# Optimization experiments

Measured on AMD Instinct MI355X. Metric: run time of the kernel, lower is better.

The kernel has to match this reference:

```python
import jax, jax.numpy as jnp
import numpy as np

B, LQ, LD, H, DIM, PF = 16, 64, 2048, 1024, 128, 4
MAXK = LD // PF + 1  # static upper bound on num clusters (valid_len <= LD)


def setup_inputs() -> dict:
    key = jax.random.key(0)
    k1, k2, k3, k4 = jax.random.split(key, 4)
    return {
        "q_hidden": jax.random.normal(k1, (B, LQ, H), jnp.float32),
        "d_hidden": jax.random.normal(k2, (B, LD, H), jnp.float32),
        "W": jax.random.normal(k3, (H, DIM), jnp.float32) * (1.0 / np.sqrt(H)),  # xavier-ish
        "b": jnp.zeros((DIM,), jnp.float32),
        "q_mask": jnp.ones((B, LQ), jnp.int32),
        "d_mask": jnp.ones((B, LD), jnp.int32),
        "labels": jax.random.randint(k4, (B, LD), 0, MAXK, dtype=jnp.int32),
        "pooling_factor": PF,
    }


def _encode(hidden, W, b, mask):
    # proj -> L2 normalize -> zero out padded tokens
    r = hidden @ W + b
    r = r / jnp.clip(jnp.linalg.norm(r, axis=-1, keepdims=True), 1e-12)
    return r * mask[..., None].astype(r.dtype)


def _pool(d_repr, d_mask, labels, pf):
    # segment-mean per batch sample, cluster labels supplied externally
    Bn, L, D = d_repr.shape
    max_k = L // pf + 1  # static
    valid = jnp.clip(d_mask.sum(-1), 2, None)          # [B]
    k = valid // pf + 1                                 # per-sample num clusters
    lab = jnp.where(d_mask > 0, labels % k[:, None], max_k)  # invalid tokens -> dummy seg
    seg = lambda vals, idx: jax.ops.segment_sum(vals, idx, num_segments=max_k + 1)
    sums = jax.vmap(seg)(d_repr, lab)[:, :max_k]                          # [B,K,D]
    counts = jax.vmap(seg)(jnp.where(d_mask > 0, 1.0, 0.0), lab)[:, :max_k]
    means = sums / jnp.clip(counts, 1.0)[..., None]
    means = means / jnp.clip(jnp.linalg.norm(means, axis=-1, keepdims=True), 1e-12)
    pad_mask = jnp.arange(max_k)[None, :] < k[:, None]                    # [B,K]
    return means * pad_mask[..., None], pad_mask


def reference(q_hidden, d_hidden, W, b, q_mask, d_mask, labels, pooling_factor):
    q = _encode(q_hidden, W, b, q_mask)            # [B,LQ,DIM]
    d = _encode(d_hidden, W, b, d_mask)            # [B,LD,DIM]
    d_pool, pmask = _pool(d, d_mask, labels, pooling_factor)  # [B,K,DIM]
    sim = jnp.einsum('bqd,bkd->bqk', q, d_pool)
    sim = jnp.where(pmask[:, None, :], sim, -1e4)
    score = (sim.max(-1) * q_mask.astype(sim.dtype)).sum(-1)  # maxsum per pair
    return score
```

## Files before the change

### kernel.cpp

```cpp
#include <hip/hip_runtime.h>
#include <hip/hip_bf16.h>

#define BB    16
#define LQ    64
#define LD    2048
#define HH    1024
#define DIM   128
#define MAXK  513
#define SCH   9
#define DGRID 512
#define QGRID 16

typedef __attribute__((ext_vector_type(8))) short short8;
typedef __attribute__((ext_vector_type(4))) float f32x4;

__device__ __forceinline__ float b2f(ushort u) {
    union { float f; unsigned int u32; } c; c.u32 = ((unsigned int)u) << 16; return c.f;
}
__device__ __forceinline__ ushort f2b_rn(float f) {
    unsigned int x = __float_as_uint(f);
    return (ushort)((x + 0x7fffu + ((x >> 16) & 1u)) >> 16);
}

__device__ __forceinline__ void gld16(void* lds, const void* g) {
    __builtin_amdgcn_global_load_lds(
        (const __attribute__((address_space(1))) unsigned int*)g,
        (__attribute__((address_space(3))) unsigned int*)lds,
        16, 0, 0);
}

__global__ __launch_bounds__(256) void prep_kb_kernel(
    const float* __restrict__ W,
    const int*   __restrict__ d_mask,
    const int*   __restrict__ pf,
    ushort*      __restrict__ Wt,
    int*         __restrict__ kvals,
    float*       __restrict__ sums)
{
    int bid = blockIdx.x, t = threadIdx.x;
    if (bid < 16) {
        __shared__ ushort tile[128][72];
        const int h0 = bid * 64;
        #pragma unroll
        for (int i = 0; i < 32; ++i) {
            int flat = i * 256 + t;
            int r = flat >> 7, c = flat & 127;
            tile[c][r] = f2b_rn(W[(long)(h0 + r) * DIM + c]);
        }
        __syncthreads();
        #pragma unroll
        for (int i = 0; i < 4; ++i) {
            int flat = i * 256 + t;
            int n = flat >> 3, u = flat & 7;
            uint4 v = *(const uint4*)&tile[n][u * 8];
            *(uint4*)&Wt[(long)n * HH + h0 + u * 8] = v;
        }
    } else if (bid < 32) {
        __shared__ int red[4];
        int b = bid - 16;
        int lane = t & 63, wave = t >> 6;
        int s = 0;
        for (int i = t; i < LD; i += 256) s += (d_mask[b * LD + i] > 0) ? 1 : 0;
        #pragma unroll
        for (int m = 1; m < 64; m <<= 1) s += __shfl_xor(s, m);
        if (lane == 0) red[wave] = s;
        __syncthreads();
        if (t == 0) {
            int v = red[0] + red[1] + red[2] + red[3];
            if (v < 2) v = 2;
            int pfv = pf[0];
            if (pfv < 1 || pfv > LD) pfv = 4;
            kvals[b] = v / pfv + 1;
        }
    } else {
        const int total4 = (BB * MAXK * DIM) / 4;
        float4* s4 = (float4*)sums;
        const float4 z = make_float4(0.f, 0.f, 0.f, 0.f);
        for (int i = (bid - 32) * 256 + t; i < total4; i += 256 * 256)
            s4[i] = z;
    }
}

__global__ __launch_bounds__(512, 6) void encode_kernel(
    const float*  __restrict__ Xd,
    const float*  __restrict__ Xq,
    const ushort* __restrict__ Wt,
    const float*  __restrict__ bias,
    const int*    __restrict__ mask_d,
    const int*    __restrict__ mask_q,
    const int*    __restrict__ labels,
    const int*    __restrict__ kvals,
    float*        __restrict__ sums,
    float*        __restrict__ q_repr)
{
    __shared__ __align__(16) uint4 buf[3][1024];
    __shared__ float ssh[64][2];

    const int bid = blockIdx.x;
    const bool isq = bid >= DGRID;
    const float* X = isq ? Xq : Xd;
    const long row0 = isq ? (long)(bid - DGRID) * 64 : (long)bid * 64;

    const int t = threadIdx.x;
    const int w = t >> 6, lane = t & 63;
    const int m16 = lane & 15, quad = lane >> 4;
    const int rh = w & 3, ch = w >> 2;

    const float*  gA = X + (row0 + w * 8 + (lane >> 3)) * HH
                         + (((lane & 7) ^ ((lane >> 3) & 7)) * 4);
    const ushort* gB = Wt + (long)(w * 16 + (lane >> 2)) * HH
                          + (((lane & 3) ^ ((lane >> 4) & 3)) * 8);

    const int wA = w * 64;
    const int wB = 512 + w * 64;

    f32x4 acc[4];
    #pragma unroll
    for (int j = 0; j < 4; ++j) acc[j] = (f32x4){0.f, 0.f, 0.f, 0.f};

    gld16(&buf[0][wA], gA);
    gld16(&buf[0][wB], gB);
    gld16(&buf[1][wA], gA + 32);
    gld16(&buf[1][wB], gB + 32);

    const int sw = m16 & 7;
    const int bsw = m16 >> 2;
    const int au = (rh * 16 + m16) * 8;

    auto compute = [&](const uint4* bb) {
        float4 va0 = *(const float4*)&bb[au + ((2 * quad) ^ sw)];
        float4 va1 = *(const float4*)&bb[au + ((2 * quad + 1) ^ sw)];
        float av[8];
        *(float4*)(av) = va0; *(float4*)(av + 4) = va1;
        short8 ah, al;
        #pragma unroll
        for (int j = 0; j < 8; ++j) {
            unsigned int ux = __float_as_uint(av[j]);
            ah[j] = (short)(ux >> 16);
            float hif = __uint_as_float(ux & 0xffff0000u);
            al[j] = (short)(__float_as_uint(av[j] - hif) >> 16);
        }
        #pragma unroll
        for (int cti = 0; cti < 4; ++cti) {
            const int ct = ch * 4 + cti;
            short8 bf = *(const short8*)&bb[512 + (ct * 16 + m16) * 4 + (quad ^ bsw)];
            acc[cti] = __builtin_amdgcn_mfma_f32_16x16x32_bf16(ah, bf, acc[cti], 0, 0, 0);
            acc[cti] = __builtin_amdgcn_mfma_f32_16x16x32_bf16(al, bf, acc[cti], 0, 0, 0);
        }
    };

    #define STEP(C, CUR, NXT)                                              \
        asm volatile("s_waitcnt vmcnt(2)" ::: "memory");                   \
        __builtin_amdgcn_s_barrier();                                      \
        __builtin_amdgcn_sched_barrier(0);                                 \
        gld16(&buf[NXT][wA], gA + ((C) + 2) * 32);                         \
        gld16(&buf[NXT][wB], gB + ((C) + 2) * 32);                         \
        compute(&buf[CUR][0]);

    for (int c = 0; c < 30; c += 3) {
        STEP(c + 0, 0, 2)
        STEP(c + 1, 1, 0)
        STEP(c + 2, 2, 1)
    }
    #undef STEP
    asm volatile("s_waitcnt vmcnt(2)" ::: "memory");
    __builtin_amdgcn_s_barrier();
    __builtin_amdgcn_sched_barrier(0);
    compute(&buf[0][0]);
    asm volatile("s_waitcnt vmcnt(0)" ::: "memory");
    __builtin_amdgcn_s_barrier();
    __builtin_amdgcn_sched_barrier(0);
    compute(&buf[1][0]);

    float bia[4];
    #pragma unroll
    for (int cti = 0; cti < 4; ++cti) bia[cti] = bias[(ch * 4 + cti) * 16 + m16];

    float vv[4][4];
    float ssp[4] = {0.f, 0.f, 0.f, 0.f};
    #pragma unroll
    for (int cti = 0; cti < 4; ++cti)
        #pragma unroll
        for (int r = 0; r < 4; ++r) {
            vv[cti][r] = acc[cti][r] + bia[cti];
            ssp[r] += vv[cti][r] * vv[cti][r];
        }
    #pragma unroll
    for (int r = 0; r < 4; ++r) {
        ssp[r] += __shfl_xor(ssp[r], 1);
        ssp[r] += __shfl_xor(ssp[r], 2);
        ssp[r] += __shfl_xor(ssp[r], 4);
        ssp[r] += __shfl_xor(ssp[r], 8);
    }
    if (m16 == 0) {
        #pragma unroll
        for (int r = 0; r < 4; ++r) ssh[rh * 16 + quad * 4 + r][ch] = ssp[r];
    }
    __syncthreads();

    #pragma unroll
    for (int r = 0; r < 4; ++r) {
        int rowl = rh * 16 + quad * 4 + r;
        long rowg = row0 + rowl;
        float ss = ssh[rowl][0] + ssh[rowl][1];
        float scale = 1.0f / fmaxf(sqrtf(ss), 1e-12f);
        if (isq) {
            scale *= (float)mask_q[rowg];
            #pragma unroll
            for (int cti = 0; cti < 4; ++cti)
                q_repr[rowg * DIM + (ch * 4 + cti) * 16 + m16] = vv[cti][r] * scale;
        } else if (mask_d[rowg] > 0) {
            int b = (int)(rowg >> 11);
            int seg = labels[rowg] % kvals[b];
            float* sp = sums + ((long)b * MAXK + seg) * DIM + m16;
            #pragma unroll
            for (int cti = 0; cti < 4; ++cti)
                atomicAdd(sp + (ch * 4 + cti) * 16, vv[cti][r] * scale);
        }
    }
}

__global__ __launch_bounds__(256) void simmax_kernel(
    const float* __restrict__ q_repr,
    const float* __restrict__ sums,
    const int*   __restrict__ kvals,
    float*       __restrict__ pmax)
{
    __shared__ __align__(16) ushort Qh[64 * 136];
    __shared__ __align__(16) ushort Ql[64 * 136];
    __shared__ __align__(16) ushort Ch[64 * 136];
    __shared__ float cn[64];

    int b = blockIdx.x / SCH, chunk = blockIdx.x % SCH;
    int t = threadIdx.x, w = t >> 6, lane = t & 63;
    int m16 = lane & 15, quad = lane >> 4;

    #pragma unroll
    for (int i = 0; i < 8; ++i) {
        int flat = i * 256 + t;
        int row = flat >> 5, c4 = flat & 31;
        float4 v = *(const float4*)(q_repr + ((long)b * LQ + row) * DIM + c4 * 4);
        float x[4]; *(float4*)x = v;
        ushort4 h, l;
        ushort* hp = (ushort*)&h; ushort* lp = (ushort*)&l;
        #pragma unroll
        for (int j = 0; j < 4; ++j) {
            unsigned int ux = __float_as_uint(x[j]);
            hp[j] = (ushort)(ux >> 16);
            lp[j] = f2b_rn(x[j] - __uint_as_float(ux & 0xffff0000u));
        }
        *(ushort4*)&Qh[row * 136 + c4 * 4] = h;
        *(ushort4*)&Ql[row * 136 + c4 * 4] = l;
    }
    #pragma unroll
    for (int i = 0; i < 8; ++i) {
        int flat = i * 256 + t;
        int row = flat >> 5, c4 = flat & 31;
        int kk = chunk * 64 + row;
        float4 v = (kk < MAXK)
            ? *(const float4*)(sums + ((long)b * MAXK + kk) * DIM + c4 * 4)
            : make_float4(0.f, 0.f, 0.f, 0.f);
        ushort4 h; ushort* hp = (ushort*)&h;
        hp[0] = f2b_rn(v.x); hp[1] = f2b_rn(v.y);
        hp[2] = f2b_rn(v.z); hp[3] = f2b_rn(v.w);
        *(ushort4*)&Ch[row * 136 + c4 * 4] = h;
    }
    __syncthreads();

    {
        int c = w * 16 + m16;
        float ssv = 0.f;
        #pragma unroll
        for (int j = 0; j < 16; ++j) {
            unsigned int u = *(const unsigned int*)&Ch[c * 136 + quad * 32 + j * 2];
            float x0 = b2f((ushort)u), x1 = b2f((ushort)(u >> 16));
            ssv += x0 * x0 + x1 * x1;
        }
        ssv += __shfl_xor(ssv, 16);
        ssv += __shfl_xor(ssv, 32);
        if (quad == 0) cn[c] = (ssv > 1e-24f) ? rsqrtf(ssv) : 0.f;
    }
    __syncthreads();

    f32x4 acc[4];
    #pragma unroll
    for (int j = 0; j < 4; ++j) acc[j] = (f32x4){0.f, 0.f, 0.f, 0.f};

    #pragma unroll
    for (int kc = 0; kc < 4; ++kc) {
        short8 qh = *(const short8*)&Qh[(w * 16 + m16) * 136 + kc * 32 + quad * 8];
        short8 ql = *(const short8*)&Ql[(w * 16 + m16) * 136 + kc * 32 + quad * 8];
        #pragma unroll
        for (int ct = 0; ct < 4; ++ct) {
            short8 cf = *(const short8*)&Ch[(ct * 16 + m16) * 136 + kc * 32 + quad * 8];
            acc[ct] = __builtin_amdgcn_mfma_f32_16x16x32_bf16(qh, cf, acc[ct], 0, 0, 0);
            acc[ct] = __builtin_amdgcn_mfma_f32_16x16x32_bf16(ql, cf, acc[ct], 0, 0, 0);
        }
    }

    int kb = kvals[b];
    #pragma unroll
    for (int r = 0; r < 4; ++r) {
        float mx = -1e4f;
        #pragma unroll
        for (int ct = 0; ct < 4; ++ct) {
            int cl = chunk * 64 + ct * 16 + m16;
            float sim = acc[ct][r] * cn[ct * 16 + m16];
            mx = fmaxf(mx, (cl < kb) ? sim : -1e4f);
        }
        mx = fmaxf(mx, __shfl_xor(mx, 1));
        mx = fmaxf(mx, __shfl_xor(mx, 2));
        mx = fmaxf(mx, __shfl_xor(mx, 4));
        mx = fmaxf(mx, __shfl_xor(mx, 8));
        if (m16 == 0)
            pmax[((long)b * SCH + chunk) * 64 + w * 16 + quad * 4 + r] = mx;
    }
}

__global__ __launch_bounds__(64) void final_kernel(
    const float* __restrict__ pmax,
    const int*   __restrict__ q_mask,
    float*       __restrict__ out)
{
    int b = blockIdx.x, r = threadIdx.x;
    float m = -3e38f;
    #pragma unroll
    for (int c = 0; c < SCH; ++c)
        m = fmaxf(m, pmax[((long)b * SCH + c) * 64 + r]);
    m *= (float)q_mask[b * LQ + r];
    #pragma unroll
    for (int sh = 1; sh < 64; sh <<= 1) m += __shfl_xor(m, sh);
    if (r == 0) out[b] = m;
}

extern "C" void kernel_launch(void* const* d_in, const int* in_sizes, int n_in,
                              void* d_out, int out_size, void* d_ws, size_t ws_size,
                              hipStream_t stream) {
    const float* q_hidden = (const float*)d_in[0];
    const float* d_hidden = (const float*)d_in[1];
    const float* W        = (const float*)d_in[2];
    const float* bias     = (const float*)d_in[3];
    const int*   q_mask   = (const int*)d_in[4];
    const int*   d_mask   = (const int*)d_in[5];
    const int*   labels   = (const int*)d_in[6];
    const int*   pf       = (const int*)d_in[7];

    float* ws     = (float*)d_ws;
    float* q_repr = ws;
    float* sums   = q_repr + (long)BB * LQ * DIM;
    float* pmaxb  = sums + (long)BB * MAXK * DIM;
    int*   kvals  = (int*)(pmaxb + BB * SCH * 64);
    ushort* Wt    = (ushort*)(kvals + 16);

    prep_kb_kernel<<<288, 256, 0, stream>>>(W, d_mask, pf, Wt, kvals, sums);
    encode_kernel<<<DGRID + QGRID, 512, 0, stream>>>(d_hidden, q_hidden, Wt, bias,
                                                     d_mask, q_mask, labels, kvals,
                                                     sums, q_repr);
    simmax_kernel<<<BB * SCH, 256, 0, stream>>>(q_repr, sums, kvals, pmaxb);
    final_kernel<<<BB, 64, 0, stream>>>(pmaxb, q_mask, (float*)d_out);
}
```

Measured before the change: 254.9 us.

## Restructure encode GEMM: per-wave 16-row units with full-width W staged in LDS

The encode kernel now gives each wave a 16-row unit that covers all 128 output columns. The block stages a quarter of the bf16 weight matrix in 64KB of LDS at a time, while A rows stream straight from global into a three-deep register prefetch instead of going through LDS. This lets each split-hi/lo conversion of A feed 8 column tiles instead of 4, and drops the cross-wave norm reduction through shared memory along with most barriers. In exchange, half the waves only help load W and do no math, LDS use grows, which may lower occupancy, and the direct global A loads are less coalesced.

Measured after the change: 247.0 us. 3.1% less time.

```diff
diff --git a/kernel.cpp b/kernel.cpp
--- a/kernel.cpp
+++ b/kernel.cpp
@@ -8,8 +8,8 @@
 #define DIM   128
 #define MAXK  513
 #define SCH   9
-#define DGRID 512
-#define QGRID 16
+#define NUNITS 2112
+#define EGRID 512
 
 typedef __attribute__((ext_vector_type(8))) short short8;
 typedef __attribute__((ext_vector_type(4))) float f32x4;
@@ -81,7 +81,7 @@
     }
 }
 
-__global__ __launch_bounds__(512, 6) void encode_kernel(
+__global__ __launch_bounds__(512, 4) void encode_kernel(
     const float*  __restrict__ Xd,
     const float*  __restrict__ Xq,
     const ushort* __restrict__ Wt,
@@ -93,97 +93,97 @@
     float*        __restrict__ sums,
     float*        __restrict__ q_repr)
 {
-    __shared__ __align__(16) uint4 buf[3][1024];
-    __shared__ float ssh[64][2];
-
-    const int bid = blockIdx.x;
-    const bool isq = bid >= DGRID;
-    const float* X = isq ? Xq : Xd;
-    const long row0 = isq ? (long)(bid - DGRID) * 64 : (long)bid * 64;
+    __shared__ __align__(16) uint4 Wlds[4096];
 
     const int t = threadIdx.x;
     const int w = t >> 6, lane = t & 63;
     const int m16 = lane & 15, quad = lane >> 4;
-    const int rh = w & 3, ch = w >> 2;
-
-    const float*  gA = X + (row0 + w * 8 + (lane >> 3)) * HH
-                         + (((lane & 7) ^ ((lane >> 3) & 7)) * 4);
-    const ushort* gB = Wt + (long)(w * 16 + (lane >> 2)) * HH
-                          + (((lane & 3) ^ ((lane >> 4) & 3)) * 8);
-
-    const int wA = w * 64;
-    const int wB = 512 + w * 64;
-
-    f32x4 acc[4];
-    #pragma unroll
-    for (int j = 0; j < 4; ++j) acc[j] = (f32x4){0.f, 0.f, 0.f, 0.f};
-
-    gld16(&buf[0][wA], gA);
-    gld16(&buf[0][wB], gB);
-    gld16(&buf[1][wA], gA + 32);
-    gld16(&buf[1][wB], gB + 32);
-
-    const int sw = m16 & 7;
-    const int bsw = m16 >> 2;
-    const int au = (rh * 16 + m16) * 8;
-
-    auto compute = [&](const uint4* bb) {
-        float4 va0 = *(const float4*)&bb[au + ((2 * quad) ^ sw)];
-        float4 va1 = *(const float4*)&bb[au + ((2 * quad + 1) ^ sw)];
-        float av[8];
-        *(float4*)(av) = va0; *(float4*)(av + 4) = va1;
-        short8 ah, al;
-        #pragma unroll
-        for (int j = 0; j < 8; ++j) {
-            unsigned int ux = __float_as_uint(av[j]);
-            ah[j] = (short)(ux >> 16);
-            float hif = __uint_as_float(ux & 0xffff0000u);
-            al[j] = (short)(__float_as_uint(av[j] - hif) >> 16);
-        }
-        #pragma unroll
-        for (int cti = 0; cti < 4; ++cti) {
-            const int ct = ch * 4 + cti;
-            short8 bf = *(const short8*)&bb[512 + (ct * 16 + m16) * 4 + (quad ^ bsw)];
-            acc[cti] = __builtin_amdgcn_mfma_f32_16x16x32_bf16(ah, bf, acc[cti], 0, 0, 0);
-            acc[cti] = __builtin_amdgcn_mfma_f32_16x16x32_bf16(al, bf, acc[cti], 0, 0, 0);
-        }
-    };
-
-    #define STEP(C, CUR, NXT)                                              \
-        asm volatile("s_waitcnt vmcnt(2)" ::: "memory");                   \
-        __builtin_amdgcn_s_barrier();                                      \
-        __builtin_amdgcn_sched_barrier(0);                                 \
-        gld16(&buf[NXT][wA], gA + ((C) + 2) * 32);                         \
-        gld16(&buf[NXT][wB], gB + ((C) + 2) * 32);                         \
-        compute(&buf[CUR][0]);
-
-    for (int c = 0; c < 30; c += 3) {
-        STEP(c + 0, 0, 2)
-        STEP(c + 1, 1, 0)
-        STEP(c + 2, 2, 1)
-    }
-    #undef STEP
-    asm volatile("s_waitcnt vmcnt(2)" ::: "memory");
-    __builtin_amdgcn_s_barrier();
-    __builtin_amdgcn_sched_barrier(0);
-    compute(&buf[0][0]);
-    asm volatile("s_waitcnt vmcnt(0)" ::: "memory");
-    __builtin_amdgcn_s_barrier();
-    __builtin_amdgcn_sched_barrier(0);
-    compute(&buf[1][0]);
-
-    float bia[4];
-    #pragma unroll
-    for (int cti = 0; cti < 4; ++cti) bia[cti] = bias[(ch * 4 + cti) * 16 + m16];
-
-    float vv[4][4];
+    const int s = blockIdx.x * 8 + w;
+
+    int unit = -1;
+    if ((s & 1) == 0) unit = s >> 1;
+    else if ((s & 63) == 1) unit = 2048 + (s >> 6);
+    const bool active = unit >= 0;
+    const bool isq = unit >= 2048;
+
+    long row0 = 0;
+    const float* aptr = Xd;
+    if (active) {
+        row0 = isq ? (long)(unit - 2048) * 16 : (long)unit * 16;
+        const float* Xb = isq ? Xq : Xd;
+        aptr = Xb + (row0 + m16) * HH + quad * 8;
+    }
+
+    f32x4 acc[8];
+    #pragma unroll
+    for (int j = 0; j < 8; ++j) acc[j] = (f32x4){0.f, 0.f, 0.f, 0.f};
+
+    const int sw8 = m16 & 7;
+    const ushort* Wu = (const ushort*)Wlds;
+
+    float4 ast[3][2];
+    if (active) {
+        ast[0][0] = *(const float4*)(aptr);
+        ast[0][1] = *(const float4*)(aptr + 4);
+        ast[1][0] = *(const float4*)(aptr + 32);
+        ast[1][1] = *(const float4*)(aptr + 32 + 4);
+    }
+
+    #pragma unroll
+    for (int p = 0; p < 4; ++p) {
+        __syncthreads();
+        #pragma unroll
+        for (int i = 0; i < 8; ++i) {
+            int Si = w * 512 + i * 64 + lane;
+            int n  = Si >> 5, up = Si & 31;
+            const ushort* src = Wt + (long)n * HH + (p * 32 + (up ^ (n & 7))) * 8;
+            gld16(&Wlds[w * 512 + i * 64], src);
+        }
+        __syncthreads();
+        if (active) {
+            #pragma unroll
+            for (int cc = 0; cc < 8; ++cc) {
+                const int c = p * 8 + cc;
+                if (c + 2 < 32) {
+                    ast[(c + 2) % 3][0] = *(const float4*)(aptr + (c + 2) * 32);
+                    ast[(c + 2) % 3][1] = *(const float4*)(aptr + (c + 2) * 32 + 4);
+                }
+                float av[8];
+                *(float4*)(av)     = ast[c % 3][0];
+                *(float4*)(av + 4) = ast[c % 3][1];
+                short8 ah, al;
+                #pragma unroll
+                for (int j = 0; j < 8; ++j) {
+                    unsigned int ux = __float_as_uint(av[j]);
+                    ah[j] = (short)(ux >> 16);
+                    float hif = __uint_as_float(ux & 0xffff0000u);
+                    al[j] = (short)(__float_as_uint(av[j] - hif) >> 16);
+                }
+                #pragma unroll
+                for (int ct = 0; ct < 8; ++ct) {
+                    short8 bf = *(const short8*)
+                        &Wu[(ct * 16 + m16) * 256 + ((cc * 4 + quad) ^ sw8) * 8];
+                    acc[ct] = __builtin_amdgcn_mfma_f32_16x16x32_bf16(ah, bf, acc[ct], 0, 0, 0);
+                    acc[ct] = __builtin_amdgcn_mfma_f32_16x16x32_bf16(al, bf, acc[ct], 0, 0, 0);
+                }
+            }
+        }
+    }
+
+    if (!active) return;
+
+    float bia[8];
+    #pragma unroll
+    for (int ct = 0; ct < 8; ++ct) bia[ct] = bias[ct * 16 + m16];
+
+    float vv[8][4];
     float ssp[4] = {0.f, 0.f, 0.f, 0.f};
     #pragma unroll
-    for (int cti = 0; cti < 4; ++cti)
+    for (int ct = 0; ct < 8; ++ct)
         #pragma unroll
         for (int r = 0; r < 4; ++r) {
-            vv[cti][r] = acc[cti][r] + bia[cti];
-            ssp[r] += vv[cti][r] * vv[cti][r];
+            vv[ct][r] = acc[ct][r] + bia[ct];
+            ssp[r] += vv[ct][r] * vv[ct][r];
         }
     #pragma unroll
     for (int r = 0; r < 4; ++r) {
@@ -192,30 +192,23 @@
         ssp[r] += __shfl_xor(ssp[r], 4);
         ssp[r] += __shfl_xor(ssp[r], 8);
     }
-    if (m16 == 0) {
-        #pragma unroll
-        for (int r = 0; r < 4; ++r) ssh[rh * 16 + quad * 4 + r][ch] = ssp[r];
-    }
-    __syncthreads();
 
     #pragma unroll
     for (int r = 0; r < 4; ++r) {
-        int rowl = rh * 16 + quad * 4 + r;
-        long rowg = row0 + rowl;
-        float ss = ssh[rowl][0] + ssh[rowl][1];
-        float scale = 1.0f / fmaxf(sqrtf(ss), 1e-12f);
+        long rowg = row0 + quad * 4 + r;
+        float scale = 1.0f / fmaxf(sqrtf(ssp[r]), 1e-12f);
         if (isq) {
             scale *= (float)mask_q[rowg];
             #pragma unroll
-            for (int cti = 0; cti < 4; ++cti)
-                q_repr[rowg * DIM + (ch * 4 + cti) * 16 + m16] = vv[cti][r] * scale;
+            for (int ct = 0; ct < 8; ++ct)
+                q_repr[rowg * DIM + ct * 16 + m16] = vv[ct][r] * scale;
         } else if (mask_d[rowg] > 0) {
             int b = (int)(rowg >> 11);
             int seg = labels[rowg] % kvals[b];
             float* sp = sums + ((long)b * MAXK + seg) * DIM + m16;
             #pragma unroll
-            for (int cti = 0; cti < 4; ++cti)
-                atomicAdd(sp + (ch * 4 + cti) * 16, vv[cti][r] * scale);
+            for (int ct = 0; ct < 8; ++ct)
+                atomicAdd(sp + ct * 16, vv[ct][r] * scale);
         }
     }
 }
@@ -353,9 +346,9 @@
     ushort* Wt    = (ushort*)(kvals + 16);
 
     prep_kb_kernel<<<288, 256, 0, stream>>>(W, d_mask, pf, Wt, kvals, sums);
-    encode_kernel<<<DGRID + QGRID, 512, 0, stream>>>(d_hidden, q_hidden, Wt, bias,
-                                                     d_mask, q_mask, labels, kvals,
-                                                     sums, q_repr);
+    encode_kernel<<<EGRID, 512, 0, stream>>>(d_hidden, q_hidden, Wt, bias,
+                                             d_mask, q_mask, labels, kvals,
+                                             sums, q_repr);
     simmax_kernel<<<BB * SCH, 256, 0, stream>>>(q_repr, sums, kvals, pmaxb);
     final_kernel<<<BB, 64, 0, stream>>>(pmaxb, q_mask, (float*)d_out);
 }
```
